# Optimization experiments

Hardware: AMD Instinct MI355X
Metric: run time of the kernel (lower is better)

## Reference

```python
import jax, jax.numpy as jnp
import numpy as np

B, L = 256, 65536
HIST, WIN = 256, 64
DIM, NPAT = 256, 64
AMP = 2.0


def setup_inputs() -> dict:
    key = jax.random.key(0)
    k1, k2, k3, k4, k5, k6 = jax.random.split(key, 6)
    x = jax.random.uniform(k1, (B, L), dtype=jnp.float32)
    avg = jax.random.uniform(k2, (B, NPAT), dtype=jnp.float32)
    avg_scores = avg - avg.mean(axis=-1, keepdims=True)
    # conv kernel (out=dim, in=1, k=history), kaiming-ish scale
    conv_w = jax.random.normal(k3, (DIM, 1, HIST), dtype=jnp.float32) * (1.0 / np.sqrt(HIST))
    conv_b = jax.random.normal(k4, (DIM,), dtype=jnp.float32) * 0.01
    # xavier-uniform keys
    lim = np.sqrt(6.0 / (DIM + NPAT))
    keys = jax.random.uniform(k5, (DIM, NPAT), minval=-lim, maxval=lim, dtype=jnp.float32)
    # shapes ~ rand * amp * 2 in [0, 4]
    shapes = jax.random.uniform(k6, (NPAT, WIN), dtype=jnp.float32) * (AMP * 2.0)
    return {"x": x, "avg_scores": avg_scores, "conv_w": conv_w, "conv_b": conv_b,
            "keys": keys, "shapes": shapes}


def reference(x, avg_scores, conv_w, conv_b, keys, shapes):
    batch, seqlen = x.shape
    n_pat = keys.shape[1]
    # Conv1d(1, dim, history, stride=window) on left-padded input, then ReLU
    # (dropout is identity at inference)
    out = jax.lax.conv_general_dilated(
        x[:, None, :], conv_w,
        window_strides=(WIN,), padding=[(HIST - 1, 0)],
        dimension_numbers=("NCH", "OIH", "NCH"))  # (B, dim, T)
    out = jax.nn.relu(out + conv_b[None, :, None])
    out = jnp.transpose(out, (2, 0, 1))  # (T, B, dim)
    # relu6(out @ keys): (T, B, n_patterns)
    attn_scores = jnp.clip(jnp.einsum("tbd,dp->tbp", out, keys), 0.0, 6.0)

    inv_p = 1.0 / n_pat

    def step(avg, score):  # avg, score: (B, n_patterns)
        prob = jax.nn.softmax(score - avg, axis=-1)
        return avg + prob - inv_p, prob

    _, probs = jax.lax.scan(step, avg_scores, attn_scores)  # probs: (T, B, P)
    attn_probs = jnp.transpose(probs, (1, 0, 2))  # (B, T, P)
    signal = jnp.einsum("btp,pw->btw", attn_probs, shapes).reshape(batch, -1)[:, :seqlen]
    return jax.nn.relu(signal - x)
```

## Files before the change

kernel.cpp:

```cpp
#include <hip/hip_runtime.h>

#define BB 256
#define LL 65536
#define TS 1024
#define HIST 256
#define WINW 64
#define DIM 256
#define NPAT 64

typedef short s8v __attribute__((ext_vector_type(8)));
typedef float f4v __attribute__((ext_vector_type(4)));

#define MFMA16(a, b, c) __builtin_amdgcn_mfma_f32_16x16x32_bf16((a), (b), (c), 0, 0, 0)
#define LOG2E 1.44269504f

__device__ __forceinline__ short bf16rne(float f) {
    unsigned u = __float_as_uint(f);
    unsigned r = (u + 0x7fffu + ((u >> 16) & 1u)) >> 16;
    return (short)r;
}
__device__ __forceinline__ float bf16tof(short h) {
    return __uint_as_float(((unsigned)(unsigned short)h) << 16);
}
__device__ __forceinline__ void split2(float f, short& hi, short& lo) {
    hi = bf16rne(f);
    lo = bf16rne(f - bf16tof(hi));
}

__global__ void prep_all(const float* __restrict__ w, short* __restrict__ wFH,
                         short* __restrict__ wFL,
                         const float* __restrict__ keys, short* __restrict__ kFH,
                         short* __restrict__ kFL,
                         const float* __restrict__ sh, short* __restrict__ sFH,
                         short* __restrict__ sFL) {
    int bid = blockIdx.x;
    s8v hv, lv;
    if (bid < 32) {
        int idx = bid * 256 + threadIdx.x;
        int d = idx & 255, qk = idx >> 8;
        int h0 = qk * 8;
#pragma unroll
        for (int j = 0; j < 8; ++j) {
            short h, l; split2(w[d * HIST + h0 + j], h, l);
            hv[j] = h; lv[j] = l;
        }
        *(s8v*)(wFH + (size_t)idx * 8) = hv;
        *(s8v*)(wFL + (size_t)idx * 8) = lv;
    } else if (bid < 40) {
        int idx = (bid - 32) * 256 + threadIdx.x;
        int p = idx & 63, qk = idx >> 6;
        int d0 = qk * 8;
#pragma unroll
        for (int j = 0; j < 8; ++j) {
            short h, l; split2(keys[(d0 + j) * NPAT + p], h, l);
            hv[j] = h; lv[j] = l;
        }
        *(s8v*)(kFH + (size_t)idx * 8) = hv;
        *(s8v*)(kFL + (size_t)idx * 8) = lv;
    } else {
        int idx = (bid - 40) * 256 + threadIdx.x;
        int ww = idx & 63, qk = idx >> 6;
        int p0 = qk * 8;
#pragma unroll
        for (int j = 0; j < 8; ++j) {
            short h, l; split2(sh[(p0 + j) * WINW + ww], h, l);
            hv[j] = h; lv[j] = l;
        }
        *(s8v*)(sFH + (size_t)idx * 8) = hv;
        *(s8v*)(sFL + (size_t)idx * 8) = lv;
    }
}

#define WELEM 2240

__device__ __forceinline__ int swz(int u) { return u ^ ((u >> 3) & 7); }

__launch_bounds__(256, 5)
__global__ void scores_mfma(const float* __restrict__ x,
                            const short* __restrict__ wFH, const short* __restrict__ wFL,
                            const short* __restrict__ kFH, const short* __restrict__ kFL,
                            const float* __restrict__ conv_b,
                            float* __restrict__ scoresT) {
    __shared__ __align__(16) short hidH[32 * 256], hidL[32 * 256];
    short* xsH = hidH;
    short* xsL = hidL;

    const int b = blockIdx.y, t0 = blockIdx.x * 32;
    const int tid = threadIdx.x;
    const int lane = tid & 63, wid = tid >> 6;
    const int m = lane & 15, q = lane >> 4;

    const float* xb = x + (size_t)b * LL;
    const int gbase = t0 * WINW - (HIST - 1);
    for (int i = tid; i < WELEM; i += 256) {
        int gi = gbase + i;
        float v = (gi >= 0) ? xb[gi] : 0.0f;
        short h, l; split2(v, h, l);
        int pos = (swz(i >> 3) << 3) | (i & 7);
        xsH[pos] = h; xsL[pos] = l;
    }
    __syncthreads();

    const int nb = wid * 64;
    f4v acc[2][4];
#pragma unroll
    for (int mt = 0; mt < 2; ++mt)
#pragma unroll
        for (int nt = 0; nt < 4; ++nt) acc[mt][nt] = (f4v)0.0f;

    for (int kt = 0; kt < 8; ++kt) {
        s8v aH[2], aL[2];
#pragma unroll
        for (int mt = 0; mt < 2; ++mt) {
            int row = mt * 16 + m;
            int su = swz(row * 8 + kt * 4 + q) << 3;
            aH[mt] = *(const s8v*)&xsH[su];
            aL[mt] = *(const s8v*)&xsL[su];
        }
        s8v bH[4], bL[4];
#pragma unroll
        for (int nt = 0; nt < 4; ++nt) {
            size_t bi = ((size_t)(kt * 4 + q) * 256 + nb + nt * 16 + m) * 8;
            bH[nt] = *(const s8v*)(wFH + bi);
            bL[nt] = *(const s8v*)(wFL + bi);
        }
#pragma unroll
        for (int mt = 0; mt < 2; ++mt)
#pragma unroll
            for (int nt = 0; nt < 4; ++nt)
                acc[mt][nt] = MFMA16(aH[mt], bH[nt], acc[mt][nt]);
#pragma unroll
        for (int mt = 0; mt < 2; ++mt)
#pragma unroll
            for (int nt = 0; nt < 4; ++nt)
                acc[mt][nt] = MFMA16(aL[mt], bH[nt], acc[mt][nt]);
#pragma unroll
        for (int mt = 0; mt < 2; ++mt)
#pragma unroll
            for (int nt = 0; nt < 4; ++nt)
                acc[mt][nt] = MFMA16(aH[mt], bL[nt], acc[mt][nt]);
    }
    __syncthreads();

#pragma unroll
    for (int mt = 0; mt < 2; ++mt)
#pragma unroll
        for (int nt = 0; nt < 4; ++nt) {
            int d = nb + nt * 16 + m;
            float bias = conv_b[d];
#pragma unroll
            for (int r = 0; r < 4; ++r) {
                int row = mt * 16 + q * 4 + r;
                float v = fmaxf(acc[mt][nt][r] + bias, 0.0f);
                short h, l; split2(v, h, l);
                int dd = d ^ ((row & 7) << 3);
                hidH[row * 256 + dd] = h;
                hidL[row * 256 + dd] = l;
            }
        }
    __syncthreads();

    const int pb = wid * 16;
    const int sw0 = (m & 7) << 3;
    f4v aHH[2], aLH[2], aHL[2];
#pragma unroll
    for (int mt = 0; mt < 2; ++mt) {
        aHH[mt] = (f4v)0.0f; aLH[mt] = (f4v)0.0f; aHL[mt] = (f4v)0.0f;
    }
    for (int kt = 0; kt < 8; ++kt) {
        s8v aH[2], aL[2];
#pragma unroll
        for (int mt = 0; mt < 2; ++mt) {
            int off = (mt * 16 + m) * 256 + ((kt * 32 + q * 8) ^ sw0);
            aH[mt] = *(const s8v*)&hidH[off];
            aL[mt] = *(const s8v*)&hidL[off];
        }
        size_t bi = ((size_t)(kt * 4 + q) * 64 + pb + m) * 8;
        s8v bH = *(const s8v*)(kFH + bi);
        s8v bL = *(const s8v*)(kFL + bi);
#pragma unroll
        for (int mt = 0; mt < 2; ++mt)
            aHH[mt] = MFMA16(aH[mt], bH, aHH[mt]);
#pragma unroll
        for (int mt = 0; mt < 2; ++mt)
            aLH[mt] = MFMA16(aL[mt], bH, aLH[mt]);
#pragma unroll
        for (int mt = 0; mt < 2; ++mt)
            aHL[mt] = MFMA16(aH[mt], bL, aHL[mt]);
    }
#pragma unroll
    for (int mt = 0; mt < 2; ++mt) {
        f4v s = aHH[mt] + aLH[mt] + aHL[mt];
        float4 st;
        st.x = fminf(fmaxf(s[0], 0.0f), 6.0f) * LOG2E;
        st.y = fminf(fmaxf(s[1], 0.0f), 6.0f) * LOG2E;
        st.z = fminf(fmaxf(s[2], 0.0f), 6.0f) * LOG2E;
        st.w = fminf(fmaxf(s[3], 0.0f), 6.0f) * LOG2E;
        *(float4*)&scoresT[((size_t)b * NPAT + pb + m) * TS + t0 + mt * 16 + q * 4] = st;
    }
}

template <int CTRL>
__device__ __forceinline__ float dppadd(float x) {
    int t = __builtin_amdgcn_update_dpp(0, __float_as_int(x), CTRL, 0xf, 0xf, true);
    return x + __int_as_float(t);
}

#define CHUNK 64
#define NCHUNK (TS / CHUNK)

__launch_bounds__(128, 1)
__global__ void scan_signal(const float* __restrict__ scoresT,
                            const float* __restrict__ avg0,
                            const short* __restrict__ sFH, const short* __restrict__ sFL,
                            const float* __restrict__ x,
                            float* __restrict__ out) {
    __shared__ __align__(16) short pbH[2][CHUNK][64], pbL[2][CHUNK][64];

    const int b = blockIdx.x;
    const int tid = threadIdx.x;
    const int wid = tid >> 6, lane = tid & 63;

    if (wid == 0) {
        const int p = lane;
        const float4* sc = (const float4*)(scoresT + ((size_t)b * NPAT + p) * TS);
        float avg = avg0[b * NPAT + p] * LOG2E;
        const float invc = LOG2E / NPAT;

        float4 buf[4];
#pragma unroll
        for (int s = 0; s < 4; ++s) buf[s] = sc[s];

        for (int c = 0; c < NCHUNK; ++c) {
            short* bH = &pbH[c & 1][0][0];
            short* bL = &pbL[c & 1][0][0];
            for (int kb = 0; kb < 16; kb += 4) {
#pragma unroll
                for (int s = 0; s < 4; ++s) {
                    const int k = kb + s;
                    const int g = c * 16 + k;
                    float4 v = buf[s];
                    float* a = (float*)&v;
#pragma unroll
                    for (int j = 0; j < 4; ++j) {
                        float e = exp2f(a[j] - avg);
                        float w = e;
                        w = dppadd<0x111>(w);
                        w = dppadd<0x112>(w);
                        w = dppadd<0x114>(w);
                        w = dppadd<0x118>(w);
                        w = dppadd<0x142>(w);
                        w = dppadd<0x143>(w);
                        float t = __int_as_float(
                            __builtin_amdgcn_readlane(__float_as_int(w), 63));
                        float pr = e * __builtin_amdgcn_rcpf(t);
                        avg = __builtin_fmaf(pr, LOG2E, avg - invc);
                        short h, l; split2(pr, h, l);
                        const int trow = k * 4 + j;
                        const int col = p ^ ((trow & 7) << 3);
                        bH[trow * 64 + col] = h;
                        bL[trow * 64 + col] = l;
                    }
                    if (g + 4 < TS / 4) buf[s] = sc[g + 4];
                }
            }
            __syncthreads();
        }
        __syncthreads();
    } else {
        const int m = lane & 15, q = lane >> 4;
        s8v sbH[2][4], sbL[2][4];
#pragma unroll
        for (int kt = 0; kt < 2; ++kt)
#pragma unroll
            for (int nt = 0; nt < 4; ++nt) {
                size_t bi = ((size_t)(kt * 4 + q) * 64 + nt * 16 + m) * 8;
                sbH[kt][nt] = *(const s8v*)(sFH + bi);
                sbL[kt][nt] = *(const s8v*)(sFL + bi);
            }
        const float* xb = x + (size_t)b * LL;
        float* ob = out + (size_t)b * LL;

        __syncthreads();
        for (int cc = 0; cc < NCHUNK; ++cc) {
            const short* pH = &pbH[cc & 1][0][0];
            const short* pL = &pbL[cc & 1][0][0];
            const int t0 = cc * CHUNK;
#pragma unroll
            for (int mt = 0; mt < 4; ++mt) {
                float xv[4][4];
#pragma unroll
                for (int nt = 0; nt < 4; ++nt)
#pragma unroll
                    for (int r = 0; r < 4; ++r)
                        xv[nt][r] = xb[(size_t)(t0 + mt * 16 + q * 4 + r) * WINW +
                                       nt * 16 + m];
                f4v acc[4];
#pragma unroll
                for (int nt = 0; nt < 4; ++nt) acc[nt] = (f4v)0.0f;
#pragma unroll
                for (int kt = 0; kt < 2; ++kt) {
                    const int rr = mt * 16 + m;
                    const int col = (kt * 32 + q * 8) ^ ((m & 7) << 3);
                    s8v aH = *(const s8v*)&pH[rr * 64 + col];
                    s8v aL = *(const s8v*)&pL[rr * 64 + col];
#pragma unroll
                    for (int nt = 0; nt < 4; ++nt) {
                        acc[nt] = MFMA16(aH, sbH[kt][nt], acc[nt]);
                        acc[nt] = MFMA16(aL, sbH[kt][nt], acc[nt]);
                        acc[nt] = MFMA16(aH, sbL[kt][nt], acc[nt]);
                    }
                }
#pragma unroll
                for (int nt = 0; nt < 4; ++nt)
#pragma unroll
                    for (int r = 0; r < 4; ++r) {
                        size_t gi = (size_t)(t0 + mt * 16 + q * 4 + r) * WINW +
                                    nt * 16 + m;
                        ob[gi] = fmaxf(acc[nt][r] - xv[nt][r], 0.0f);
                    }
            }
            __syncthreads();
        }
    }
}

extern "C" void kernel_launch(void* const* d_in, const int* in_sizes, int n_in,
                              void* d_out, int out_size, void* d_ws, size_t ws_size,
                              hipStream_t stream) {
    const float* x      = (const float*)d_in[0];
    const float* avg0   = (const float*)d_in[1];
    const float* conv_w = (const float*)d_in[2];
    const float* conv_b = (const float*)d_in[3];
    const float* keys   = (const float*)d_in[4];
    const float* shapes = (const float*)d_in[5];
    float* out = (float*)d_out;

    char* ws = (char*)d_ws;
    size_t o = 0;
    float* scoresT = (float*)(ws + o); o += (size_t)BB * TS * NPAT * 4;
    short* wFH = (short*)(ws + o); o += 8192 * 16;
    short* wFL = (short*)(ws + o); o += 8192 * 16;
    short* kFH = (short*)(ws + o); o += 2048 * 16;
    short* kFL = (short*)(ws + o); o += 2048 * 16;
    short* sFH = (short*)(ws + o); o += 512 * 16;
    short* sFL = (short*)(ws + o); o += 512 * 16;

    prep_all<<<42, 256, 0, stream>>>(conv_w, wFH, wFL, keys, kFH, kFL, shapes, sFH, sFL);
    scores_mfma<<<dim3(TS / 32, BB), 256, 0, stream>>>(x, wFH, wFL, kFH, kFL, conv_b, scoresT);
    scan_signal<<<dim3(BB), 128, 0, stream>>>(scoresT, avg0, sFH, sFL, x, out);
}
```

Measured before the change: 431.7 us.

## Fuse conv scores, softmax scan and signal into one warp-specialized pipelined kernel

Replaces the separate scores kernel and scan/signal kernel with one kernel per batch row. Four waves compute the conv and keys projection for 32-step chunks, one wave runs the serial softmax scan, and one wave produces the output signal. Scores and probabilities are passed through double-buffered shared memory in a three-stage pipeline instead of a global scoresT buffer. This removes the 64 MB scores round trip and a kernel launch, and overlaps the conv GEMMs with the serial scan. In exchange, the grid drops to 256 blocks and each chunk adds several block-wide barriers.

```diff
diff --git a/kernel.cpp b/kernel.cpp
--- a/kernel.cpp
+++ b/kernel.cpp
@@ -75,23 +75,15 @@
 
 __device__ __forceinline__ int swz(int u) { return u ^ ((u >> 3) & 7); }
 
-__launch_bounds__(256, 5)
-__global__ void scores_mfma(const float* __restrict__ x,
-                            const short* __restrict__ wFH, const short* __restrict__ wFL,
-                            const short* __restrict__ kFH, const short* __restrict__ kFL,
-                            const float* __restrict__ conv_b,
-                            float* __restrict__ scoresT) {
-    __shared__ __align__(16) short hidH[32 * 256], hidL[32 * 256];
-    short* xsH = hidH;
-    short* xsL = hidL;
-
-    const int b = blockIdx.y, t0 = blockIdx.x * 32;
-    const int tid = threadIdx.x;
-    const int lane = tid & 63, wid = tid >> 6;
-    const int m = lane & 15, q = lane >> 4;
-
-    const float* xb = x + (size_t)b * LL;
-    const int gbase = t0 * WINW - (HIST - 1);
+template <int CTRL>
+__device__ __forceinline__ float dppadd(float x) {
+    int t = __builtin_amdgcn_update_dpp(0, __float_as_int(x), CTRL, 0xf, 0xf, true);
+    return x + __int_as_float(t);
+}
+
+__device__ __forceinline__ void stage_xs(short* xsH, short* xsL,
+                                         const float* __restrict__ xb, int c, int tid) {
+    const int gbase = c * 32 * WINW - (HIST - 1);
     for (int i = tid; i < WELEM; i += 256) {
         int gi = gbase + i;
         float v = (gi >= 0) ? xb[gi] : 0.0f;
@@ -99,229 +91,242 @@
         int pos = (swz(i >> 3) << 3) | (i & 7);
         xsH[pos] = h; xsL[pos] = l;
     }
-    __syncthreads();
-
-    const int nb = wid * 64;
-    f4v acc[2][4];
-#pragma unroll
-    for (int mt = 0; mt < 2; ++mt)
-#pragma unroll
-        for (int nt = 0; nt < 4; ++nt) acc[mt][nt] = (f4v)0.0f;
-
-    for (int kt = 0; kt < 8; ++kt) {
-        s8v aH[2], aL[2];
-#pragma unroll
-        for (int mt = 0; mt < 2; ++mt) {
-            int row = mt * 16 + m;
-            int su = swz(row * 8 + kt * 4 + q) << 3;
-            aH[mt] = *(const s8v*)&xsH[su];
-            aL[mt] = *(const s8v*)&xsL[su];
-        }
-        s8v bH[4], bL[4];
-#pragma unroll
-        for (int nt = 0; nt < 4; ++nt) {
-            size_t bi = ((size_t)(kt * 4 + q) * 256 + nb + nt * 16 + m) * 8;
-            bH[nt] = *(const s8v*)(wFH + bi);
-            bL[nt] = *(const s8v*)(wFL + bi);
-        }
-#pragma unroll
-        for (int mt = 0; mt < 2; ++mt)
-#pragma unroll
-            for (int nt = 0; nt < 4; ++nt)
-                acc[mt][nt] = MFMA16(aH[mt], bH[nt], acc[mt][nt]);
-#pragma unroll
-        for (int mt = 0; mt < 2; ++mt)
-#pragma unroll
-            for (int nt = 0; nt < 4; ++nt)
-                acc[mt][nt] = MFMA16(aL[mt], bH[nt], acc[mt][nt]);
-#pragma unroll
-        for (int mt = 0; mt < 2; ++mt)
-#pragma unroll
-            for (int nt = 0; nt < 4; ++nt)
-                acc[mt][nt] = MFMA16(aH[mt], bL[nt], acc[mt][nt]);
+}
+
+template <int N>
+__device__ __forceinline__ void scan_seg(const float* srow,
+                                         int p, short* bH, short* bL,
+                                         int k0, float& avg) {
+    const float invc = LOG2E / NPAT;
+    float sreg[N];
+#pragma unroll
+    for (int i = 0; i < N; ++i) sreg[i] = srow[(k0 + i) * 64 + p];
+#pragma unroll
+    for (int i = 0; i < N; ++i) {
+        float e = exp2f(sreg[i] - avg);
+        float w = e;
+        w = dppadd<0x111>(w);
+        w = dppadd<0x112>(w);
+        w = dppadd<0x114>(w);
+        w = dppadd<0x118>(w);
+        w = dppadd<0x142>(w);
+        w = dppadd<0x143>(w);
+        float t = __int_as_float(__builtin_amdgcn_readlane(__float_as_int(w), 63));
+        float pr = e * __builtin_amdgcn_rcpf(t);
+        avg = __builtin_fmaf(pr, LOG2E, avg - invc);
+        short h, l; split2(pr, h, l);
+        const int trow = k0 + i;
+        const int col = p ^ ((trow & 7) << 3);
+        bH[trow * 64 + col] = h;
+        bL[trow * 64 + col] = l;
     }
-    __syncthreads();
-
-#pragma unroll
-    for (int mt = 0; mt < 2; ++mt)
-#pragma unroll
-        for (int nt = 0; nt < 4; ++nt) {
-            int d = nb + nt * 16 + m;
-            float bias = conv_b[d];
-#pragma unroll
-            for (int r = 0; r < 4; ++r) {
-                int row = mt * 16 + q * 4 + r;
-                float v = fmaxf(acc[mt][nt][r] + bias, 0.0f);
-                short h, l; split2(v, h, l);
-                int dd = d ^ ((row & 7) << 3);
-                hidH[row * 256 + dd] = h;
-                hidL[row * 256 + dd] = l;
-            }
-        }
-    __syncthreads();
-
-    const int pb = wid * 16;
-    const int sw0 = (m & 7) << 3;
-    f4v aHH[2], aLH[2], aHL[2];
-#pragma unroll
-    for (int mt = 0; mt < 2; ++mt) {
-        aHH[mt] = (f4v)0.0f; aLH[mt] = (f4v)0.0f; aHL[mt] = (f4v)0.0f;
-    }
-    for (int kt = 0; kt < 8; ++kt) {
-        s8v aH[2], aL[2];
-#pragma unroll
-        for (int mt = 0; mt < 2; ++mt) {
-            int off = (mt * 16 + m) * 256 + ((kt * 32 + q * 8) ^ sw0);
-            aH[mt] = *(const s8v*)&hidH[off];
-            aL[mt] = *(const s8v*)&hidL[off];
-        }
-        size_t bi = ((size_t)(kt * 4 + q) * 64 + pb + m) * 8;
-        s8v bH = *(const s8v*)(kFH + bi);
-        s8v bL = *(const s8v*)(kFL + bi);
-#pragma unroll
-        for (int mt = 0; mt < 2; ++mt)
-            aHH[mt] = MFMA16(aH[mt], bH, aHH[mt]);
-#pragma unroll
-        for (int mt = 0; mt < 2; ++mt)
-            aLH[mt] = MFMA16(aL[mt], bH, aLH[mt]);
-#pragma unroll
-        for (int mt = 0; mt < 2; ++mt)
-            aHL[mt] = MFMA16(aH[mt], bL, aHL[mt]);
-    }
-#pragma unroll
-    for (int mt = 0; mt < 2; ++mt) {
-        f4v s = aHH[mt] + aLH[mt] + aHL[mt];
-        float4 st;
-        st.x = fminf(fmaxf(s[0], 0.0f), 6.0f) * LOG2E;
-        st.y = fminf(fmaxf(s[1], 0.0f), 6.0f) * LOG2E;
-        st.z = fminf(fmaxf(s[2], 0.0f), 6.0f) * LOG2E;
-        st.w = fminf(fmaxf(s[3], 0.0f), 6.0f) * LOG2E;
-        *(float4*)&scoresT[((size_t)b * NPAT + pb + m) * TS + t0 + mt * 16 + q * 4] = st;
-    }
-}
-
-template <int CTRL>
-__device__ __forceinline__ float dppadd(float x) {
-    int t = __builtin_amdgcn_update_dpp(0, __float_as_int(x), CTRL, 0xf, 0xf, true);
-    return x + __int_as_float(t);
-}
-
-#define CHUNK 64
-#define NCHUNK (TS / CHUNK)
-
-__launch_bounds__(128, 1)
-__global__ void scan_signal(const float* __restrict__ scoresT,
-                            const float* __restrict__ avg0,
-                            const short* __restrict__ sFH, const short* __restrict__ sFL,
-                            const float* __restrict__ x,
-                            float* __restrict__ out) {
-    __shared__ __align__(16) short pbH[2][CHUNK][64], pbL[2][CHUNK][64];
+}
+
+__launch_bounds__(384, 1)
+__global__ void fused_pipeline(const float* __restrict__ x,
+                               const short* __restrict__ wFH, const short* __restrict__ wFL,
+                               const short* __restrict__ kFH, const short* __restrict__ kFL,
+                               const short* __restrict__ sFH, const short* __restrict__ sFL,
+                               const float* __restrict__ conv_b,
+                               const float* __restrict__ avg0,
+                               float* __restrict__ out) {
+    __shared__ __align__(16) short hidH[32 * 256], hidL[32 * 256];
+    __shared__ __align__(16) float scoresL[2][32 * 64];
+    __shared__ __align__(16) short pbH[2][32 * 64], pbL[2][32 * 64];
+    short* xsH = hidH;
+    short* xsL = hidL;
 
     const int b = blockIdx.x;
     const int tid = threadIdx.x;
     const int wid = tid >> 6, lane = tid & 63;
-
-    if (wid == 0) {
-        const int p = lane;
-        const float4* sc = (const float4*)(scoresT + ((size_t)b * NPAT + p) * TS);
-        float avg = avg0[b * NPAT + p] * LOG2E;
-        const float invc = LOG2E / NPAT;
-
-        float4 buf[4];
-#pragma unroll
-        for (int s = 0; s < 4; ++s) buf[s] = sc[s];
-
-        for (int c = 0; c < NCHUNK; ++c) {
-            short* bH = &pbH[c & 1][0][0];
-            short* bL = &pbL[c & 1][0][0];
-            for (int kb = 0; kb < 16; kb += 4) {
-#pragma unroll
-                for (int s = 0; s < 4; ++s) {
-                    const int k = kb + s;
-                    const int g = c * 16 + k;
-                    float4 v = buf[s];
-                    float* a = (float*)&v;
-#pragma unroll
-                    for (int j = 0; j < 4; ++j) {
-                        float e = exp2f(a[j] - avg);
-                        float w = e;
-                        w = dppadd<0x111>(w);
-                        w = dppadd<0x112>(w);
-                        w = dppadd<0x114>(w);
-                        w = dppadd<0x118>(w);
-                        w = dppadd<0x142>(w);
-                        w = dppadd<0x143>(w);
-                        float t = __int_as_float(
-                            __builtin_amdgcn_readlane(__float_as_int(w), 63));
-                        float pr = e * __builtin_amdgcn_rcpf(t);
-                        avg = __builtin_fmaf(pr, LOG2E, avg - invc);
-                        short h, l; split2(pr, h, l);
-                        const int trow = k * 4 + j;
-                        const int col = p ^ ((trow & 7) << 3);
-                        bH[trow * 64 + col] = h;
-                        bL[trow * 64 + col] = l;
-                    }
-                    if (g + 4 < TS / 4) buf[s] = sc[g + 4];
+    const int m = lane & 15, q = lane >> 4;
+    const float* xb = x + (size_t)b * LL;
+    float* ob = out + (size_t)b * LL;
+
+    float avg = 0.0f;
+    if (wid == 4) avg = avg0[b * NPAT + lane] * LOG2E;
+
+    if (wid < 4) stage_xs(xsH, xsL, xb, 0, tid);
+
+    for (int c = 0; c < 34; ++c) {
+        f4v acc[2][4];
+
+        __syncthreads();
+        if (wid < 4) {
+            if (c < 32) {
+                const int nb = wid * 64;
+#pragma unroll
+                for (int mt = 0; mt < 2; ++mt)
+#pragma unroll
+                    for (int nt = 0; nt < 4; ++nt) acc[mt][nt] = (f4v)0.0f;
+                for (int kt = 0; kt < 8; ++kt) {
+                    s8v aH[2], aL[2];
+#pragma unroll
+                    for (int mt = 0; mt < 2; ++mt) {
+                        int row = mt * 16 + m;
+                        int su = swz(row * 8 + kt * 4 + q) << 3;
+                        aH[mt] = *(const s8v*)&xsH[su];
+                        aL[mt] = *(const s8v*)&xsL[su];
+                    }
+                    s8v bH[4], bL[4];
+#pragma unroll
+                    for (int nt = 0; nt < 4; ++nt) {
+                        size_t bi = ((size_t)(kt * 4 + q) * 256 + nb + nt * 16 + m) * 8;
+                        bH[nt] = *(const s8v*)(wFH + bi);
+                        bL[nt] = *(const s8v*)(wFL + bi);
+                    }
+#pragma unroll
+                    for (int mt = 0; mt < 2; ++mt)
+#pragma unroll
+                        for (int nt = 0; nt < 4; ++nt)
+                            acc[mt][nt] = MFMA16(aH[mt], bH[nt], acc[mt][nt]);
+#pragma unroll
+                    for (int mt = 0; mt < 2; ++mt)
+#pragma unroll
+                        for (int nt = 0; nt < 4; ++nt)
+                            acc[mt][nt] = MFMA16(aL[mt], bH[nt], acc[mt][nt]);
+#pragma unroll
+                    for (int mt = 0; mt < 2; ++mt)
+#pragma unroll
+                        for (int nt = 0; nt < 4; ++nt)
+                            acc[mt][nt] = MFMA16(aH[mt], bL[nt], acc[mt][nt]);
                 }
             }
-            __syncthreads();
-        }
+        } else if (wid == 4) {
+            if (c >= 1 && c <= 32)
+                scan_seg<12>(scoresL[(c - 1) & 1], lane, pbH[(c - 1) & 1],
+                             pbL[(c - 1) & 1], 0, avg);
+        } else {
+            if (c >= 2) {
+                const int cs = c - 2;
+                const int t0 = cs * 32;
+                const short* pH = pbH[cs & 1];
+                const short* pL = pbL[cs & 1];
+                s8v sbH[2][4], sbL[2][4];
+#pragma unroll
+                for (int kt = 0; kt < 2; ++kt)
+#pragma unroll
+                    for (int nt = 0; nt < 4; ++nt) {
+                        size_t bi = ((size_t)(kt * 4 + q) * 64 + nt * 16 + m) * 8;
+                        sbH[kt][nt] = *(const s8v*)(sFH + bi);
+                        sbL[kt][nt] = *(const s8v*)(sFL + bi);
+                    }
+#pragma unroll
+                for (int mt = 0; mt < 2; ++mt) {
+                    float xv[4][4];
+#pragma unroll
+                    for (int nt = 0; nt < 4; ++nt)
+#pragma unroll
+                        for (int r = 0; r < 4; ++r)
+                            xv[nt][r] = xb[(size_t)(t0 + mt * 16 + q * 4 + r) * WINW +
+                                           nt * 16 + m];
+                    f4v acc2[4];
+#pragma unroll
+                    for (int nt = 0; nt < 4; ++nt) acc2[nt] = (f4v)0.0f;
+#pragma unroll
+                    for (int kt = 0; kt < 2; ++kt) {
+                        const int rr = mt * 16 + m;
+                        const int col = (kt * 32 + q * 8) ^ ((m & 7) << 3);
+                        s8v aH = *(const s8v*)&pH[rr * 64 + col];
+                        s8v aL = *(const s8v*)&pL[rr * 64 + col];
+#pragma unroll
+                        for (int nt = 0; nt < 4; ++nt) {
+                            acc2[nt] = MFMA16(aH, sbH[kt][nt], acc2[nt]);
+                            acc2[nt] = MFMA16(aL, sbH[kt][nt], acc2[nt]);
+                            acc2[nt] = MFMA16(aH, sbL[kt][nt], acc2[nt]);
+                        }
+                    }
+#pragma unroll
+                    for (int nt = 0; nt < 4; ++nt)
+#pragma unroll
+                        for (int r = 0; r < 4; ++r) {
+                            size_t gi = (size_t)(t0 + mt * 16 + q * 4 + r) * WINW +
+                                        nt * 16 + m;
+                            ob[gi] = fmaxf(acc2[nt][r] - xv[nt][r], 0.0f);
+                        }
+                }
+            }
+        }
+
         __syncthreads();
-    } else {
-        const int m = lane & 15, q = lane >> 4;
-        s8v sbH[2][4], sbL[2][4];
-#pragma unroll
-        for (int kt = 0; kt < 2; ++kt)
-#pragma unroll
-            for (int nt = 0; nt < 4; ++nt) {
-                size_t bi = ((size_t)(kt * 4 + q) * 64 + nt * 16 + m) * 8;
-                sbH[kt][nt] = *(const s8v*)(sFH + bi);
-                sbL[kt][nt] = *(const s8v*)(sFL + bi);
+        if (wid < 4) {
+            if (c < 32) {
+                const int nb = wid * 64;
+#pragma unroll
+                for (int mt = 0; mt < 2; ++mt)
+#pragma unroll
+                    for (int nt = 0; nt < 4; ++nt) {
+                        int d = nb + nt * 16 + m;
+                        float bias = conv_b[d];
+#pragma unroll
+                        for (int r = 0; r < 4; ++r) {
+                            int row = mt * 16 + q * 4 + r;
+                            float v = fmaxf(acc[mt][nt][r] + bias, 0.0f);
+                            short h, l; split2(v, h, l);
+                            int dd = d ^ ((row & 7) << 3);
+                            hidH[row * 256 + dd] = h;
+                            hidL[row * 256 + dd] = l;
+                        }
+                    }
             }
-        const float* xb = x + (size_t)b * LL;
-        float* ob = out + (size_t)b * LL;
+        } else if (wid == 4) {
+            if (c >= 1 && c <= 32)
+                scan_seg<10>(scoresL[(c - 1) & 1], lane, pbH[(c - 1) & 1],
+                             pbL[(c - 1) & 1], 12, avg);
+        }
 
         __syncthreads();
-        for (int cc = 0; cc < NCHUNK; ++cc) {
-            const short* pH = &pbH[cc & 1][0][0];
-            const short* pL = &pbL[cc & 1][0][0];
-            const int t0 = cc * CHUNK;
-#pragma unroll
-            for (int mt = 0; mt < 4; ++mt) {
-                float xv[4][4];
-#pragma unroll
-                for (int nt = 0; nt < 4; ++nt)
-#pragma unroll
-                    for (int r = 0; r < 4; ++r)
-                        xv[nt][r] = xb[(size_t)(t0 + mt * 16 + q * 4 + r) * WINW +
-                                       nt * 16 + m];
-                f4v acc[4];
-#pragma unroll
-                for (int nt = 0; nt < 4; ++nt) acc[nt] = (f4v)0.0f;
-#pragma unroll
-                for (int kt = 0; kt < 2; ++kt) {
-                    const int rr = mt * 16 + m;
-                    const int col = (kt * 32 + q * 8) ^ ((m & 7) << 3);
-                    s8v aH = *(const s8v*)&pH[rr * 64 + col];
-                    s8v aL = *(const s8v*)&pL[rr * 64 + col];
-#pragma unroll
-                    for (int nt = 0; nt < 4; ++nt) {
-                        acc[nt] = MFMA16(aH, sbH[kt][nt], acc[nt]);
-                        acc[nt] = MFMA16(aL, sbH[kt][nt], acc[nt]);
-                        acc[nt] = MFMA16(aH, sbL[kt][nt], acc[nt]);
-                    }
-                }
-#pragma unroll
-                for (int nt = 0; nt < 4; ++nt)
+        if (wid < 4) {
+            if (c < 32) {
+                const int pb = wid * 16;
+                const int sw0 = (m & 7) << 3;
+                f4v aHH[2], aLH[2], aHL[2];
+#pragma unroll
+                for (int mt = 0; mt < 2; ++mt) {
+                    aHH[mt] = (f4v)0.0f; aLH[mt] = (f4v)0.0f; aHL[mt] = (f4v)0.0f;
+                }
+                for (int kt = 0; kt < 8; ++kt) {
+                    s8v aH[2], aL[2];
+#pragma unroll
+                    for (int mt = 0; mt < 2; ++mt) {
+                        int off = (mt * 16 + m) * 256 + ((kt * 32 + q * 8) ^ sw0);
+                        aH[mt] = *(const s8v*)&hidH[off];
+                        aL[mt] = *(const s8v*)&hidL[off];
+                    }
+                    size_t bi = ((size_t)(kt * 4 + q) * 64 + pb + m) * 8;
+                    s8v bH = *(const s8v*)(kFH + bi);
+                    s8v bL = *(const s8v*)(kFL + bi);
+#pragma unroll
+                    for (int mt = 0; mt < 2; ++mt)
+                        aHH[mt] = MFMA16(aH[mt], bH, aHH[mt]);
+#pragma unroll
+                    for (int mt = 0; mt < 2; ++mt)
+                        aLH[mt] = MFMA16(aL[mt], bH, aLH[mt]);
+#pragma unroll
+                    for (int mt = 0; mt < 2; ++mt)
+                        aHL[mt] = MFMA16(aH[mt], bL, aHL[mt]);
+                }
+                float* sdst = scoresL[c & 1];
+#pragma unroll
+                for (int mt = 0; mt < 2; ++mt) {
+                    f4v s = aHH[mt] + aLH[mt] + aHL[mt];
 #pragma unroll
                     for (int r = 0; r < 4; ++r) {
-                        size_t gi = (size_t)(t0 + mt * 16 + q * 4 + r) * WINW +
-                                    nt * 16 + m;
-                        ob[gi] = fmaxf(acc[nt][r] - xv[nt][r], 0.0f);
-                    }
+                        int t = mt * 16 + q * 4 + r;
+                        float v = fminf(fmaxf(s[r], 0.0f), 6.0f) * LOG2E;
+                        sdst[t * 64 + pb + m] = v;
+                    }
+                }
             }
-            __syncthreads();
-        }
+        } else if (wid == 4) {
+            if (c >= 1 && c <= 32)
+                scan_seg<10>(scoresL[(c - 1) & 1], lane, pbH[(c - 1) & 1],
+                             pbL[(c - 1) & 1], 22, avg);
+        }
+
+        __syncthreads();
+        if (wid < 4 && c < 31)
+            stage_xs(xsH, xsL, xb, c + 1, tid);
     }
 }
 
@@ -338,7 +343,6 @@
 
     char* ws = (char*)d_ws;
     size_t o = 0;
-    float* scoresT = (float*)(ws + o); o += (size_t)BB * TS * NPAT * 4;
     short* wFH = (short*)(ws + o); o += 8192 * 16;
     short* wFL = (short*)(ws + o); o += 8192 * 16;
     short* kFH = (short*)(ws + o); o += 2048 * 16;
@@ -347,6 +351,6 @@
     short* sFL = (short*)(ws + o); o += 512 * 16;
 
     prep_all<<<42, 256, 0, stream>>>(conv_w, wFH, wFL, keys, kFH, kFL, shapes, sFH, sFL);
-    scores_mfma<<<dim3(TS / 32, BB), 256, 0, stream>>>(x, wFH, wFL, kFH, kFL, conv_b, scoresT);
-    scan_signal<<<dim3(BB), 128, 0, stream>>>(scoresT, avg0, sFH, sFL, x, out);
-}
+    fused_pipeline<<<dim3(BB), 384, 0, stream>>>(x, wFH, wFL, kFH, kFL, sFH, sFL,
+                                                 conv_b, avg0, out);
+}
```

After: 729.5 us. 69.0% more time.

## Shorten serial softmax scan critical path with butterfly allreduce and precomputed next exponent

Applied to the files above, without the earlier changes.

The serial scan step now reduces the 64-lane sum with a butterfly allreduce built from row DPP adds plus permlane16/32 swaps, replacing the row-broadcast DPP chain and readlane. It also algebraically rewrites the next step's exponent argument so that only an FMA on the reciprocal sits on the dependency chain, with the rest precomputed from the next score. The scores kernel's occupancy hint drops from 5 to 4 waves. The goal is lower per-timestep latency in the latency-bound recurrence. In exchange it relies on gfx950-specific inline asm, and the reordered arithmetic may change rounding slightly.

```diff
diff --git a/kernel.cpp b/kernel.cpp
--- a/kernel.cpp
+++ b/kernel.cpp
@@ -75,7 +75,7 @@
 
 __device__ __forceinline__ int swz(int u) { return u ^ ((u >> 3) & 7); }
 
-__launch_bounds__(256, 5)
+__launch_bounds__(256, 4)
 __global__ void scores_mfma(const float* __restrict__ x,
                             const short* __restrict__ wFH, const short* __restrict__ wFL,
                             const short* __restrict__ kFH, const short* __restrict__ kFL,
@@ -206,6 +206,21 @@
     return x + __int_as_float(t);
 }
 
+__device__ __forceinline__ float allsum64(float w) {
+    w = dppadd<0x121>(w);
+    w = dppadd<0x122>(w);
+    w = dppadd<0x124>(w);
+    w = dppadd<0x128>(w);
+    float a = w, b;
+    asm("v_mov_b32 %0, %1" : "=v"(b) : "v"(a));
+    asm("v_permlane16_swap_b32 %0, %1" : "+v"(a), "+v"(b));
+    float w2 = a + b;
+    float c = w2, d;
+    asm("v_mov_b32 %0, %1" : "=v"(d) : "v"(c));
+    asm("v_permlane32_swap_b32 %0, %1" : "+v"(c), "+v"(d));
+    return c + d;
+}
+
 #define CHUNK 64
 #define NCHUNK (TS / CHUNK)
 
@@ -231,35 +246,35 @@
 #pragma unroll
         for (int s = 0; s < 4; ++s) buf[s] = sc[s];
 
+        float e = __builtin_amdgcn_exp2f(((float*)&buf[0])[0] - avg);
+
         for (int c = 0; c < NCHUNK; ++c) {
             short* bH = &pbH[c & 1][0][0];
             short* bL = &pbL[c & 1][0][0];
             for (int kb = 0; kb < 16; kb += 4) {
 #pragma unroll
                 for (int s = 0; s < 4; ++s) {
-                    const int k = kb + s;
-                    const int g = c * 16 + k;
+                    const int g = c * 16 + kb + s;
                     float4 v = buf[s];
                     float* a = (float*)&v;
+                    const float nx0 = ((float*)&buf[(s + 1) & 3])[0];
 #pragma unroll
                     for (int j = 0; j < 4; ++j) {
-                        float e = exp2f(a[j] - avg);
-                        float w = e;
-                        w = dppadd<0x111>(w);
-                        w = dppadd<0x112>(w);
-                        w = dppadd<0x114>(w);
-                        w = dppadd<0x118>(w);
-                        w = dppadd<0x142>(w);
-                        w = dppadd<0x143>(w);
-                        float t = __int_as_float(
-                            __builtin_amdgcn_readlane(__float_as_int(w), 63));
-                        float pr = e * __builtin_amdgcn_rcpf(t);
+                        const float snext = (j < 3) ? a[j + 1] : nx0;
+                        const float C = (snext + invc) - avg;
+                        const float B = e * LOG2E;
+                        const float t = allsum64(e);
+                        const float r = __builtin_amdgcn_rcpf(t);
+                        const float pr = e * r;
+                        const float xn = __builtin_fmaf(-B, r, C);
+                        const float en = __builtin_amdgcn_exp2f(xn);
                         avg = __builtin_fmaf(pr, LOG2E, avg - invc);
                         short h, l; split2(pr, h, l);
-                        const int trow = k * 4 + j;
+                        const int trow = (kb + s) * 4 + j;
                         const int col = p ^ ((trow & 7) << 3);
                         bH[trow * 64 + col] = h;
                         bL[trow * 64 + col] = l;
+                        e = en;
                     }
                     if (g + 4 < TS / 4) buf[s] = sc[g + 4];
                 }
```

Measured after the change: 429.4 us. Within noise of the previous version (-0.5%).

## Interleave two batch scans per wave to hide serial softmax latency

Applied to the files above, without the earlier changes.

The scan kernel now has one producer wave run two independent batch recurrences interleaved, so the DPP reduction and readlane latency chains of one batch overlap with the other's. Two consumer waves each compute the signal for one batch, and the chunk size is halved to keep LDS within limits. The grid drops to half as many blocks. The scores kernel's launch-bounds occupancy hint is lowered from 5 to 4, which gives the compiler more registers but allows fewer resident blocks.

```diff
diff --git a/kernel.cpp b/kernel.cpp
--- a/kernel.cpp
+++ b/kernel.cpp
@@ -75,7 +75,7 @@
 
 __device__ __forceinline__ int swz(int u) { return u ^ ((u >> 3) & 7); }
 
-__launch_bounds__(256, 5)
+__launch_bounds__(256, 4)
 __global__ void scores_mfma(const float* __restrict__ x,
                             const short* __restrict__ wFH, const short* __restrict__ wFL,
                             const short* __restrict__ kFH, const short* __restrict__ kFL,
@@ -206,69 +206,92 @@
     return x + __int_as_float(t);
 }
 
-#define CHUNK 64
-#define NCHUNK (TS / CHUNK)
-
-__launch_bounds__(128, 1)
-__global__ void scan_signal(const float* __restrict__ scoresT,
-                            const float* __restrict__ avg0,
-                            const short* __restrict__ sFH, const short* __restrict__ sFL,
-                            const float* __restrict__ x,
-                            float* __restrict__ out) {
-    __shared__ __align__(16) short pbH[2][CHUNK][64], pbL[2][CHUNK][64];
-
-    const int b = blockIdx.x;
+#define CH 32
+#define NCH (TS / CH)
+#define SLOT (CH * 64)
+
+__launch_bounds__(192, 1)
+__global__ void scan_signal2(const float* __restrict__ scoresT,
+                             const float* __restrict__ avg0,
+                             const short* __restrict__ sFH, const short* __restrict__ sFL,
+                             const float* __restrict__ x,
+                             float* __restrict__ out) {
+    __shared__ __align__(16) short pbAH[2 * SLOT], pbAL[2 * SLOT];
+    __shared__ __align__(16) short pbBH[2 * SLOT], pbBL[2 * SLOT];
+
+    const int blk = blockIdx.x;
+    const int bA = 2 * blk, bB = 2 * blk + 1;
     const int tid = threadIdx.x;
     const int wid = tid >> 6, lane = tid & 63;
 
     if (wid == 0) {
         const int p = lane;
-        const float4* sc = (const float4*)(scoresT + ((size_t)b * NPAT + p) * TS);
-        float avg = avg0[b * NPAT + p] * LOG2E;
+        const float4* sA = (const float4*)(scoresT + ((size_t)bA * NPAT + p) * TS);
+        const float4* sB = (const float4*)(scoresT + ((size_t)bB * NPAT + p) * TS);
+        float avgA = avg0[bA * NPAT + p] * LOG2E;
+        float avgB = avg0[bB * NPAT + p] * LOG2E;
         const float invc = LOG2E / NPAT;
 
-        float4 buf[4];
-#pragma unroll
-        for (int s = 0; s < 4; ++s) buf[s] = sc[s];
-
-        for (int c = 0; c < NCHUNK; ++c) {
-            short* bH = &pbH[c & 1][0][0];
-            short* bL = &pbL[c & 1][0][0];
-            for (int kb = 0; kb < 16; kb += 4) {
+        float4 bufA[4], bufB[4];
+#pragma unroll
+        for (int s = 0; s < 4; ++s) { bufA[s] = sA[s]; bufB[s] = sB[s]; }
+
+        for (int c = 0; c < NCH; ++c) {
+            short* bHA = pbAH + (c & 1) * SLOT;
+            short* bLA = pbAL + (c & 1) * SLOT;
+            short* bHB = pbBH + (c & 1) * SLOT;
+            short* bLB = pbBL + (c & 1) * SLOT;
+            for (int kb = 0; kb < 8; kb += 4) {
 #pragma unroll
                 for (int s = 0; s < 4; ++s) {
-                    const int k = kb + s;
-                    const int g = c * 16 + k;
-                    float4 v = buf[s];
-                    float* a = (float*)&v;
+                    const int g = c * 8 + kb + s;
+                    float4 vA = bufA[s], vB = bufB[s];
+                    float* a = (float*)&vA;
+                    float* bv = (float*)&vB;
 #pragma unroll
                     for (int j = 0; j < 4; ++j) {
-                        float e = exp2f(a[j] - avg);
-                        float w = e;
-                        w = dppadd<0x111>(w);
-                        w = dppadd<0x112>(w);
-                        w = dppadd<0x114>(w);
-                        w = dppadd<0x118>(w);
-                        w = dppadd<0x142>(w);
-                        w = dppadd<0x143>(w);
-                        float t = __int_as_float(
-                            __builtin_amdgcn_readlane(__float_as_int(w), 63));
-                        float pr = e * __builtin_amdgcn_rcpf(t);
-                        avg = __builtin_fmaf(pr, LOG2E, avg - invc);
-                        short h, l; split2(pr, h, l);
-                        const int trow = k * 4 + j;
+                        float eA = exp2f(a[j] - avgA);
+                        float eB = exp2f(bv[j] - avgB);
+                        float wA = eA, wB = eB;
+                        wA = dppadd<0x111>(wA); wB = dppadd<0x111>(wB);
+                        wA = dppadd<0x112>(wA); wB = dppadd<0x112>(wB);
+                        wA = dppadd<0x114>(wA); wB = dppadd<0x114>(wB);
+                        wA = dppadd<0x118>(wA); wB = dppadd<0x118>(wB);
+                        wA = dppadd<0x142>(wA); wB = dppadd<0x142>(wB);
+                        wA = dppadd<0x143>(wA); wB = dppadd<0x143>(wB);
+                        float tA = __int_as_float(
+                            __builtin_amdgcn_readlane(__float_as_int(wA), 63));
+                        float tB = __int_as_float(
+                            __builtin_amdgcn_readlane(__float_as_int(wB), 63));
+                        float prA = eA * __builtin_amdgcn_rcpf(tA);
+                        float prB = eB * __builtin_amdgcn_rcpf(tB);
+                        avgA = __builtin_fmaf(prA, LOG2E, avgA - invc);
+                        avgB = __builtin_fmaf(prB, LOG2E, avgB - invc);
+                        const int trow = (kb + s) * 4 + j;
                         const int col = p ^ ((trow & 7) << 3);
-                        bH[trow * 64 + col] = h;
-                        bL[trow * 64 + col] = l;
+                        short h, l;
+                        split2(prA, h, l);
+                        bHA[trow * 64 + col] = h;
+                        bLA[trow * 64 + col] = l;
+                        split2(prB, h, l);
+                        bHB[trow * 64 + col] = h;
+                        bLB[trow * 64 + col] = l;
                     }
-                    if (g + 4 < TS / 4) buf[s] = sc[g + 4];
+                    if (g + 4 < TS / 4) {
+                        bufA[s] = sA[g + 4];
+                        bufB[s] = sB[g + 4];
+                    }
                 }
             }
             __syncthreads();
         }
         __syncthreads();
     } else {
+        const int b = (wid == 1) ? bA : bB;
+        const short* rbH = (wid == 1) ? pbAH : pbBH;
+        const short* rbL = (wid == 1) ? pbAL : pbBL;
         const int m = lane & 15, q = lane >> 4;
+
         s8v sbH[2][4], sbL[2][4];
 #pragma unroll
         for (int kt = 0; kt < 2; ++kt)
@@ -282,12 +305,12 @@
         float* ob = out + (size_t)b * LL;
 
         __syncthreads();
-        for (int cc = 0; cc < NCHUNK; ++cc) {
-            const short* pH = &pbH[cc & 1][0][0];
-            const short* pL = &pbL[cc & 1][0][0];
-            const int t0 = cc * CHUNK;
-#pragma unroll
-            for (int mt = 0; mt < 4; ++mt) {
+        for (int cc = 0; cc < NCH; ++cc) {
+            const short* pH = rbH + (cc & 1) * SLOT;
+            const short* pL = rbL + (cc & 1) * SLOT;
+            const int t0 = cc * CH;
+#pragma unroll
+            for (int mt = 0; mt < 2; ++mt) {
                 float xv[4][4];
 #pragma unroll
                 for (int nt = 0; nt < 4; ++nt)
@@ -348,5 +371,5 @@
 
     prep_all<<<42, 256, 0, stream>>>(conv_w, wFH, wFL, keys, kFH, kFL, shapes, sFH, sFL);
     scores_mfma<<<dim3(TS / 32, BB), 256, 0, stream>>>(x, wFH, wFL, kFH, kFL, conv_b, scoresT);
-    scan_signal<<<dim3(BB), 128, 0, stream>>>(scoresT, avg0, sFH, sFL, x, out);
-}
+    scan_signal2<<<dim3(BB / 2), 192, 0, stream>>>(scoresT, avg0, sFH, sFL, x, out);
+}
```

After: 384.6 us. 1.12x faster.
